# Kernel optimization log

Measured on AMD Instinct MI355X. Metric: run time of the kernel, lower is better.

The kernel has to match this reference:

```python
import jax, jax.numpy as jnp
import numpy as np

N_HEAD = 16
NEG_INF = -1e9  # matches the original's -1000000000.0 mask fill


def setup_inputs() -> dict:
    key = jax.random.key(0)
    k1, k2, k3 = jax.random.split(key, 3)
    n_embd = 1024
    b, t = 2, 2048
    x = jax.random.normal(k1, (b, t, n_embd), dtype=jnp.float32)
    w_attn = jax.random.normal(k2, (n_embd, 3 * n_embd), dtype=jnp.float32) * 0.02
    b_attn = jnp.zeros((3 * n_embd,), dtype=jnp.float32)
    w_proj = jax.random.normal(k3, (n_embd, n_embd), dtype=jnp.float32) * 0.02
    b_proj = jnp.zeros((n_embd,), dtype=jnp.float32)
    return {"x": x, "w_attn": w_attn, "b_attn": b_attn, "w_proj": w_proj, "b_proj": b_proj}


def reference(x, w_attn, b_attn, w_proj, b_proj):
    b, t, c = x.shape
    hd = c // N_HEAD
    scale = 1.0 / np.sqrt(hd)
    qkv = x @ w_attn + b_attn                        # [b, t, 3c]
    q, k, v = jnp.split(qkv, 3, axis=-1)
    # split heads -> [b, nh, t, hd]
    def heads(z):
        return z.reshape(b, t, N_HEAD, hd).transpose(0, 2, 1, 3)
    q, k, v = heads(q), heads(k), heads(v)
    att = jnp.einsum('bhqd,bhkd->bhqk', q, k) * scale  # [b, nh, t, t]
    mask = jnp.tril(jnp.ones((t, t), dtype=bool))
    att = jnp.where(mask[None, None], att, jnp.float32(NEG_INF))
    att = jax.nn.softmax(att, axis=-1)
    y = jnp.einsum('bhqk,bhkd->bhqd', att, v)          # [b, nh, t, hd]
    y = y.transpose(0, 2, 1, 3).reshape(b, t, c)
    return y @ w_proj + b_proj
```

## Files before the change

### kernel.cpp

```cpp
#include <hip/hip_runtime.h>
#include <hip/hip_bf16.h>
#include <math.h>

typedef __attribute__((ext_vector_type(8))) short short8;
typedef __attribute__((ext_vector_type(4))) float f32x4;
typedef unsigned short u16;

static __device__ __forceinline__ u16 f2bf(float f) {
  union { float f; unsigned u; } v; v.f = f;
  unsigned r = v.u + 0x7fffu + ((v.u >> 16) & 1u);
  return (u16)(r >> 16);
}

static __device__ __forceinline__ float bf2f(u16 h) {
  union { unsigned u; float f; } v; v.u = ((unsigned)h) << 16;
  return v.f;
}

static __device__ __forceinline__ void gload_lds16(const void* g, void* l) {
  __builtin_amdgcn_global_load_lds(
      (const __attribute__((address_space(1))) void*)g,
      (__attribute__((address_space(3))) void*)l, 16, 0, 0);
}

__global__ __launch_bounds__(256) void cvt_bf16(const float* __restrict__ in,
                                                u16* __restrict__ out, int n) {
  int i = (blockIdx.x * 256 + threadIdx.x) * 8;
  if (i >= n) return;
  float4 a = *(const float4*)(in + i);
  float4 b = *(const float4*)(in + i + 4);
  uint4 pk;
  pk.x = f2bf(a.x) | ((unsigned)f2bf(a.y) << 16);
  pk.y = f2bf(a.z) | ((unsigned)f2bf(a.w) << 16);
  pk.z = f2bf(b.x) | ((unsigned)f2bf(b.y) << 16);
  pk.w = f2bf(b.z) | ((unsigned)f2bf(b.w) << 16);
  *(uint4*)(out + i) = pk;
}

template<int KD, int ND>
__global__ __launch_bounds__(256) void transpose_bf16(const float* __restrict__ W,
                                                      u16* __restrict__ WT) {
  __shared__ float tile[64][65];
  const int c0 = blockIdx.x * 64;
  const int k0 = blockIdx.y * 64;
  const int t = threadIdx.x;
  const int lr = t >> 2;
  const int lc = (t & 3) * 16;
  const float* src = W + (size_t)(k0 + lr) * ND + c0 + lc;
#pragma unroll
  for (int i = 0; i < 16; i += 4) {
    float4 v = *(const float4*)(src + i);
    tile[lr][lc + i] = v.x; tile[lr][lc + i + 1] = v.y;
    tile[lr][lc + i + 2] = v.z; tile[lr][lc + i + 3] = v.w;
  }
  __syncthreads();
  unsigned pk[8];
#pragma unroll
  for (int j = 0; j < 8; ++j) {
    u16 lo = f2bf(tile[lc + 2 * j][lr]);
    u16 hi = f2bf(tile[lc + 2 * j + 1][lr]);
    pk[j] = lo | ((unsigned)hi << 16);
  }
  u16* dst = WT + (size_t)(c0 + lr) * KD + k0 + lc;
  *(uint4*)(dst) = make_uint4(pk[0], pk[1], pk[2], pk[3]);
  *(uint4*)(dst + 8) = make_uint4(pk[4], pk[5], pk[6], pk[7]);
}

template<int NSIZE, int MODE>
__global__ __launch_bounds__(256) void gemm_bt(const u16* __restrict__ A,
                                               const u16* __restrict__ Bt,
                                               const float* __restrict__ bias,
                                               u16* __restrict__ qb,
                                               u16* __restrict__ kb,
                                               u16* __restrict__ vb,
                                               float* __restrict__ outp) {
  constexpr int K = 1024;
  __shared__ u16 As[128 * 64];
  __shared__ u16 Bs[128 * 64];
  const int tid = threadIdx.x;
  const int lane = tid & 63;
  const int wid = tid >> 6;
  const int l15 = lane & 15;
  const int g4 = lane >> 4;
  const int wm = (wid >> 1) * 64;
  const int wn = (wid & 1) * 64;
  const int row0 = blockIdx.x * 128;
  const int col0 = blockIdx.y * 128;

  f32x4 acc[4][4] = {};

  const int srow = tid >> 3;
  const int sblk = (tid & 7) ^ (srow & 7);
  const u16* ga = A + (size_t)(row0 + srow) * K + sblk * 8;
  const u16* gb = Bt + (size_t)(col0 + srow) * K + sblk * 8;
  u16* la = As + tid * 8;
  u16* lb = Bs + tid * 8;

  for (int kt = 0; kt < K / 64; ++kt) {
#pragma unroll
    for (int i = 0; i < 4; ++i) {
      gload_lds16(ga + (size_t)i * 32 * K + kt * 64, la + i * 2048);
      gload_lds16(gb + (size_t)i * 32 * K + kt * 64, lb + i * 2048);
    }
    __syncthreads();
#pragma unroll
    for (int ks = 0; ks < 2; ++ks) {
      short8 af[4], bf[4];
      const int B = ks * 64 + g4 * 16;
      const int sw = (l15 & 7) << 4;
#pragma unroll
      for (int mt = 0; mt < 4; ++mt)
        af[mt] = *(const short8*)((const char*)As + (wm + mt * 16 + l15) * 128 + (B ^ sw));
#pragma unroll
      for (int nt = 0; nt < 4; ++nt)
        bf[nt] = *(const short8*)((const char*)Bs + (wn + nt * 16 + l15) * 128 + (B ^ sw));
#pragma unroll
      for (int mt = 0; mt < 4; ++mt)
#pragma unroll
        for (int nt = 0; nt < 4; ++nt)
          acc[mt][nt] = __builtin_amdgcn_mfma_f32_16x16x32_bf16(af[mt], bf[nt], acc[mt][nt], 0, 0, 0);
    }
    __syncthreads();
  }

#pragma unroll
  for (int nt = 0; nt < 4; ++nt) {
    const int col = col0 + wn + nt * 16 + l15;
    const float bv = bias[col];
    if (MODE == 0) {
      const int part = col >> 10;
      const int h = (col >> 6) & 15;
      const int d = col & 63;
      u16* dp = part == 0 ? qb : kb;
#pragma unroll
      for (int mt = 0; mt < 4; ++mt) {
        if (part == 2) {
          const int t0 = row0 + wm + mt * 16 + g4 * 4;
          const int bidx = t0 >> 11;
          const int tt = t0 & 2047;
          const unsigned lo = f2bf(acc[mt][nt][0] + bv) | ((unsigned)f2bf(acc[mt][nt][1] + bv) << 16);
          const unsigned hi = f2bf(acc[mt][nt][2] + bv) | ((unsigned)f2bf(acc[mt][nt][3] + bv) << 16);
          *(uint2*)&vb[((size_t)((bidx << 4) + h) * 64 + d) * 2048 + tt] = make_uint2(lo, hi);
        } else {
#pragma unroll
          for (int r = 0; r < 4; ++r) {
            const int row = row0 + wm + mt * 16 + g4 * 4 + r;
            const int bidx = row >> 11;
            const int tt = row & 2047;
            dp[((size_t)((bidx << 4) + h) * 2048 + tt) * 64 + d] = f2bf(acc[mt][nt][r] + bv);
          }
        }
      }
    } else {
#pragma unroll
      for (int mt = 0; mt < 4; ++mt) {
#pragma unroll
        for (int r = 0; r < 4; ++r) {
          const int row = row0 + wm + mt * 16 + g4 * 4 + r;
          outp[(size_t)row * NSIZE + col] = acc[mt][nt][r] + bv;
        }
      }
    }
  }
}

__global__ __launch_bounds__(256, 3) void attn_fwd(const u16* __restrict__ Qb,
                                                   const u16* __restrict__ Kb,
                                                   const u16* __restrict__ Vtb,
                                                   u16* __restrict__ Yb,
                                                   char* __restrict__ pb) {
  __shared__ u16 Ks[2][64 * 64];
  __shared__ u16 Vs[2][64 * 64];
  __shared__ u16 Ps[4][2048];
  const int bh = blockIdx.x;
  const int y = blockIdx.y;
  int j, c0t, c1t, chunk, split;
  if (y < 8)       { j = 8 + y;  c0t = 0;  c1t = 15;        chunk = 0; split = 1; }
  else if (y < 16) { j = 15 - y; c0t = 0;  c1t = 2 * j + 1; chunk = 0; split = 0; }
  else             { j = y - 8;  c0t = 16; c1t = 2 * j + 1; chunk = 1; split = 1; }
  const int q0 = j * 128;
  const int tid = threadIdx.x;
  const int lane = tid & 63;
  const int wid = tid >> 6;
  const int l15 = lane & 15;
  const int g4 = lane >> 4;
  const size_t bhq = (size_t)bh * 2048 * 64;
  const u16* Kbase = Kb + bhq;
  const u16* Vbase = Vtb + bhq;
  const float C2 = 0.18033688011112042f;
  u16* Pw = &Ps[wid][0];
  const int wrow0 = q0 + wid * 32;

  short8 ones;
#pragma unroll
  for (int i = 0; i < 8; ++i) ones[i] = (short)0x3F80;

  short8 qf[2][2];
#pragma unroll
  for (int g = 0; g < 2; ++g) {
    const u16* qp = Qb + bhq + (size_t)(wrow0 + g * 16 + l15) * 64 + g4 * 8;
    qf[g][0] = *(const short8*)(qp);
    qf[g][1] = *(const short8*)(qp + 32);
  }
  f32x4 accy[2][4] = {};
  float m_q[2] = {-1e30f, -1e30f};
  float m_r[2][4] = {{-1e30f, -1e30f, -1e30f, -1e30f}, {-1e30f, -1e30f, -1e30f, -1e30f}};
  float l_r[2][4] = {};

  int cur = 0;
#pragma unroll
  for (int cc = 0; cc < 2; ++cc) {
    const int c = tid + cc * 256;
    const int srow = c >> 3;
    const int sblk = (c & 7) ^ (srow & 7);
    gload_lds16(Kbase + (size_t)(c0t * 64 + srow) * 64 + sblk * 8, Ks[0] + c * 8);
    gload_lds16(Vbase + (size_t)srow * 2048 + c0t * 64 + sblk * 8, Vs[0] + c * 8);
  }

  for (int kv = c0t; kv <= c1t; ++kv) {
    const int kv0 = kv * 64;
    if (kv < c1t) {
      const int nx0 = kv0 + 64;
#pragma unroll
      for (int cc = 0; cc < 2; ++cc) {
        const int c = tid + cc * 256;
        const int srow = c >> 3;
        const int sblk = (c & 7) ^ (srow & 7);
        gload_lds16(Kbase + (size_t)(nx0 + srow) * 64 + sblk * 8, Ks[cur ^ 1] + c * 8);
        gload_lds16(Vbase + (size_t)srow * 2048 + nx0 + sblk * 8, Vs[cur ^ 1] + c * 8);
      }
      asm volatile("s_waitcnt vmcnt(4)" ::: "memory");
    } else {
      asm volatile("s_waitcnt vmcnt(0)" ::: "memory");
    }
    __builtin_amdgcn_s_barrier();
    asm volatile("" ::: "memory");

    if (kv0 <= wrow0 + 31) {
      const u16* Kt = Ks[cur];
      const u16* Vt = Vs[cur];

      f32x4 s[2][4];
#pragma unroll
      for (int nt = 0; nt < 4; ++nt) {
        const int R = nt * 16 + l15;
        const int sw = (R & 7) << 4;
        short8 kf0 = *(const short8*)((const char*)Kt + R * 128 + ((g4 * 16) ^ sw));
        short8 kf1 = *(const short8*)((const char*)Kt + R * 128 + ((64 + g4 * 16) ^ sw));
        f32x4 z0 = __builtin_amdgcn_mfma_f32_16x16x32_bf16(kf0, qf[0][0], f32x4{}, 0, 0, 0);
        s[0][nt] = __builtin_amdgcn_mfma_f32_16x16x32_bf16(kf1, qf[0][1], z0, 0, 0, 0);
        f32x4 z1 = __builtin_amdgcn_mfma_f32_16x16x32_bf16(kf0, qf[1][0], f32x4{}, 0, 0, 0);
        s[1][nt] = __builtin_amdgcn_mfma_f32_16x16x32_bf16(kf1, qf[1][1], z1, 0, 0, 0);
      }

#pragma unroll
      for (int g = 0; g < 2; ++g) {
        const int grow0 = wrow0 + g * 16;
        if (kv0 + 63 > grow0) {
          const int qg = grow0 + l15;
#pragma unroll
          for (int nt = 0; nt < 4; ++nt) {
            const int kbase = kv0 + nt * 16 + g4 * 4;
#pragma unroll
            for (int r = 0; r < 4; ++r)
              if (kbase + r > qg) s[g][nt][r] = -1e30f;
          }
        }
        float mx = fmaxf(fmaxf(fmaxf(s[g][0][0], s[g][0][1]), fmaxf(s[g][0][2], s[g][0][3])),
                         fmaxf(fmaxf(s[g][1][0], s[g][1][1]), fmaxf(s[g][1][2], s[g][1][3])));
        mx = fmaxf(mx, fmaxf(fmaxf(fmaxf(s[g][2][0], s[g][2][1]), fmaxf(s[g][2][2], s[g][2][3])),
                             fmaxf(fmaxf(s[g][3][0], s[g][3][1]), fmaxf(s[g][3][2], s[g][3][3]))));
        mx = fmaxf(mx, __shfl_xor(mx, 16));
        mx = fmaxf(mx, __shfl_xor(mx, 32));
        if (!__all(mx <= m_q[g] + 44.0f)) {
          m_q[g] = fmaxf(m_q[g], mx);
#pragma unroll
          for (int rr = 0; rr < 4; ++rr) {
            const float mn = __shfl(m_q[g], g4 * 4 + rr);
            const float al = __builtin_amdgcn_exp2f((m_r[g][rr] - mn) * C2);
            m_r[g][rr] = mn;
            l_r[g][rr] *= al;
#pragma unroll
            for (int nt = 0; nt < 4; ++nt) accy[g][nt][rr] *= al;
          }
        }
        const float m2 = m_q[g] * C2;
#pragma unroll
        for (int nt = 0; nt < 4; ++nt)
#pragma unroll
          for (int r = 0; r < 4; ++r)
            s[g][nt][r] = __builtin_amdgcn_exp2f(fmaf(s[g][nt][r], C2, -m2));

#pragma unroll
        for (int nt = 0; nt < 4; ++nt) {
          const unsigned lo = f2bf(s[g][nt][0]) | ((unsigned)f2bf(s[g][nt][1]) << 16);
          const unsigned hi = f2bf(s[g][nt][2]) | ((unsigned)f2bf(s[g][nt][3]) << 16);
          const int rowL = g * 16 + l15;
          const int colB = nt * 32 + g4 * 8;
          *(uint2*)((char*)Pw + rowL * 128 + (colB ^ ((rowL & 7) << 4))) = make_uint2(lo, hi);
        }
      }

      short8 pf[2][2];
#pragma unroll
      for (int g = 0; g < 2; ++g) {
        const int rowL = g * 16 + l15;
        const int sw = (rowL & 7) << 4;
        pf[g][0] = *(const short8*)((const char*)Pw + rowL * 128 + ((g4 * 16) ^ sw));
        pf[g][1] = *(const short8*)((const char*)Pw + rowL * 128 + ((64 + g4 * 16) ^ sw));
      }
#pragma unroll
      for (int g = 0; g < 2; ++g) {
        f32x4 ps = __builtin_amdgcn_mfma_f32_16x16x32_bf16(pf[g][0], ones, f32x4{}, 0, 0, 0);
        ps = __builtin_amdgcn_mfma_f32_16x16x32_bf16(pf[g][1], ones, ps, 0, 0, 0);
#pragma unroll
        for (int rr = 0; rr < 4; ++rr) l_r[g][rr] += ps[rr];
      }
#pragma unroll
      for (int nt = 0; nt < 4; ++nt) {
        const int R = nt * 16 + l15;
        const int sw = (R & 7) << 4;
        short8 vf0 = *(const short8*)((const char*)Vt + R * 128 + ((g4 * 16) ^ sw));
        short8 vf1 = *(const short8*)((const char*)Vt + R * 128 + ((64 + g4 * 16) ^ sw));
#pragma unroll
        for (int g = 0; g < 2; ++g) {
          accy[g][nt] = __builtin_amdgcn_mfma_f32_16x16x32_bf16(pf[g][0], vf0, accy[g][nt], 0, 0, 0);
          accy[g][nt] = __builtin_amdgcn_mfma_f32_16x16x32_bf16(pf[g][1], vf1, accy[g][nt], 0, 0, 0);
        }
      }
    }

    asm volatile("" ::: "memory");
    __builtin_amdgcn_s_barrier();
    cur ^= 1;
  }

  if (!split) {
#pragma unroll
    for (int g = 0; g < 2; ++g)
#pragma unroll
      for (int r = 0; r < 4; ++r) {
        const int row = wrow0 + g * 16 + g4 * 4 + r;
        const float inv = 1.0f / l_r[g][r];
        const size_t base = ((size_t)(bh >> 4) * 2048 + row) * 1024 + (bh & 15) * 64;
#pragma unroll
        for (int nt = 0; nt < 4; ++nt)
          Yb[base + nt * 16 + l15] = f2bf(accy[g][nt][r] * inv);
      }
  } else {
    char* slot = pb + ((size_t)(bh * 8 + (j - 8)) * 2 + chunk) * 17408;
    u16* O = (u16*)slot;
    float* mf = (float*)(slot + 16384);
    float* lf = (float*)(slot + 16896);
#pragma unroll
    for (int g = 0; g < 2; ++g)
#pragma unroll
      for (int r = 0; r < 4; ++r) {
        const int row = wid * 32 + g * 16 + g4 * 4 + r;
        const float inv = 1.0f / l_r[g][r];
#pragma unroll
        for (int nt = 0; nt < 4; ++nt)
          O[row * 64 + nt * 16 + l15] = f2bf(accy[g][nt][r] * inv);
        if (l15 == 0) { mf[row] = m_r[g][r]; lf[row] = l_r[g][r]; }
      }
  }
}

__global__ __launch_bounds__(256) void attn_combine(const char* __restrict__ pb,
                                                    u16* __restrict__ Yb) {
  const int x = blockIdx.x;
  const int bh = blockIdx.y;
  const int j = 8 + (x >> 1);
  const int half = x & 1;
  const int T = 2 * j + half;
  const char* s0 = pb + ((size_t)(bh * 8 + (j - 8)) * 2) * 17408;
  const char* s1 = s0 + 17408;
  const int tid = threadIdx.x;
  const int r64 = tid >> 2;
  const int rowl = half * 64 + r64;
  const int dc = (tid & 3) * 16;
  const float C2 = 0.18033688011112042f;
  const float m0 = ((const float*)(s0 + 16384))[rowl];
  const float m1 = ((const float*)(s1 + 16384))[rowl];
  const float l0 = ((const float*)(s0 + 16896))[rowl];
  const float l1 = ((const float*)(s1 + 16896))[rowl];
  const float m = fmaxf(m0, m1);
  const float w0 = __builtin_amdgcn_exp2f((m0 - m) * C2) * l0;
  const float w1 = __builtin_amdgcn_exp2f((m1 - m) * C2) * l1;
  const float inv = 1.0f / (w0 + w1);
  const float a0 = w0 * inv, a1 = w1 * inv;
  const u16* O0 = (const u16*)s0 + rowl * 64 + dc;
  const u16* O1 = (const u16*)s1 + rowl * 64 + dc;
  const int qrow = T * 64 + r64;
  u16* yp = Yb + ((size_t)(bh >> 4) * 2048 + qrow) * 1024 + (bh & 15) * 64 + dc;
  union { uint4 v; u16 h[8]; } a[2], b[2], o[2];
  a[0].v = *(const uint4*)O0; a[1].v = *(const uint4*)(O0 + 8);
  b[0].v = *(const uint4*)O1; b[1].v = *(const uint4*)(O1 + 8);
#pragma unroll
  for (int jj = 0; jj < 2; ++jj)
#pragma unroll
    for (int i = 0; i < 8; ++i)
      o[jj].h[i] = f2bf(bf2f(a[jj].h[i]) * a0 + bf2f(b[jj].h[i]) * a1);
  *(uint4*)yp = o[0].v;
  *(uint4*)(yp + 8) = o[1].v;
}

extern "C" void kernel_launch(void* const* d_in, const int* in_sizes, int n_in,
                              void* d_out, int out_size, void* d_ws, size_t ws_size,
                              hipStream_t stream) {
  const float* x      = (const float*)d_in[0];
  const float* w_attn = (const float*)d_in[1];
  const float* b_attn = (const float*)d_in[2];
  const float* w_proj = (const float*)d_in[3];
  const float* b_proj = (const float*)d_in[4];
  float* out = (float*)d_out;
  char* ws = (char*)d_ws;

  u16* xb  = (u16*)(ws + (size_t)0);
  u16* wTa = (u16*)(ws + ((size_t)8  << 20));
  u16* wTp = (u16*)(ws + ((size_t)14 << 20));
  u16* qb  = (u16*)(ws + ((size_t)16 << 20));
  u16* kb  = (u16*)(ws + ((size_t)24 << 20));
  u16* vb  = (u16*)(ws + ((size_t)32 << 20));
  u16* yb  = (u16*)(ws + ((size_t)40 << 20));
  char* pb = ws;

  cvt_bf16<<<2048, 256, 0, stream>>>(x, xb, 2 * 2048 * 1024);
  transpose_bf16<1024, 3072><<<dim3(48, 16), 256, 0, stream>>>(w_attn, wTa);
  transpose_bf16<1024, 1024><<<dim3(16, 16), 256, 0, stream>>>(w_proj, wTp);
  gemm_bt<3072, 0><<<dim3(32, 24), 256, 0, stream>>>(xb, wTa, b_attn, qb, kb, vb, nullptr);
  attn_fwd<<<dim3(32, 24), 256, 0, stream>>>(qb, kb, vb, yb, pb);
  attn_combine<<<dim3(16, 32), 256, 0, stream>>>(pb, yb);
  gemm_bt<1024, 1><<<dim3(32, 8), 256, 0, stream>>>(yb, wTp, b_proj, nullptr, nullptr, nullptr, out);
}
```

Measured before the change: 125.2 us.

## Double-buffer LDS tiles in GEMM to overlap global loads with MFMA

```diff
diff --git a/kernel.cpp b/kernel.cpp
--- a/kernel.cpp
+++ b/kernel.cpp
@@ -75,8 +75,8 @@
                                                u16* __restrict__ vb,
                                                float* __restrict__ outp) {
   constexpr int K = 1024;
-  __shared__ u16 As[128 * 64];
-  __shared__ u16 Bs[128 * 64];
+  __shared__ u16 As[2][128 * 64];
+  __shared__ u16 Bs[2][128 * 64];
   const int tid = threadIdx.x;
   const int lane = tid & 63;
   const int wid = tid >> 6;
@@ -93,16 +93,30 @@
   const int sblk = (tid & 7) ^ (srow & 7);
   const u16* ga = A + (size_t)(row0 + srow) * K + sblk * 8;
   const u16* gb = Bt + (size_t)(col0 + srow) * K + sblk * 8;
-  u16* la = As + tid * 8;
-  u16* lb = Bs + tid * 8;
-
+
+#pragma unroll
+  for (int i = 0; i < 4; ++i) {
+    gload_lds16(ga + (size_t)i * 32 * K, As[0] + tid * 8 + i * 2048);
+    gload_lds16(gb + (size_t)i * 32 * K, Bs[0] + tid * 8 + i * 2048);
+  }
+
+  int cur = 0;
   for (int kt = 0; kt < K / 64; ++kt) {
-#pragma unroll
-    for (int i = 0; i < 4; ++i) {
-      gload_lds16(ga + (size_t)i * 32 * K + kt * 64, la + i * 2048);
-      gload_lds16(gb + (size_t)i * 32 * K + kt * 64, lb + i * 2048);
+    if (kt + 1 < K / 64) {
+#pragma unroll
+      for (int i = 0; i < 4; ++i) {
+        gload_lds16(ga + (size_t)i * 32 * K + (kt + 1) * 64, As[cur ^ 1] + tid * 8 + i * 2048);
+        gload_lds16(gb + (size_t)i * 32 * K + (kt + 1) * 64, Bs[cur ^ 1] + tid * 8 + i * 2048);
+      }
+      asm volatile("s_waitcnt vmcnt(8)" ::: "memory");
+    } else {
+      asm volatile("s_waitcnt vmcnt(0)" ::: "memory");
     }
-    __syncthreads();
+    __builtin_amdgcn_s_barrier();
+    asm volatile("" ::: "memory");
+
+    const u16* Ac = As[cur];
+    const u16* Bc = Bs[cur];
 #pragma unroll
     for (int ks = 0; ks < 2; ++ks) {
       short8 af[4], bf[4];
@@ -110,17 +124,20 @@
       const int sw = (l15 & 7) << 4;
 #pragma unroll
       for (int mt = 0; mt < 4; ++mt)
-        af[mt] = *(const short8*)((const char*)As + (wm + mt * 16 + l15) * 128 + (B ^ sw));
+        af[mt] = *(const short8*)((const char*)Ac + (wm + mt * 16 + l15) * 128 + (B ^ sw));
 #pragma unroll
       for (int nt = 0; nt < 4; ++nt)
-        bf[nt] = *(const short8*)((const char*)Bs + (wn + nt * 16 + l15) * 128 + (B ^ sw));
+        bf[nt] = *(const short8*)((const char*)Bc + (wn + nt * 16 + l15) * 128 + (B ^ sw));
 #pragma unroll
       for (int mt = 0; mt < 4; ++mt)
 #pragma unroll
         for (int nt = 0; nt < 4; ++nt)
           acc[mt][nt] = __builtin_amdgcn_mfma_f32_16x16x32_bf16(af[mt], bf[nt], acc[mt][nt], 0, 0, 0);
     }
-    __syncthreads();
+
+    asm volatile("" ::: "memory");
+    __builtin_amdgcn_s_barrier();
+    cur ^= 1;
   }
 
 #pragma unroll
```

Result: no change. 123.0 us (-1.7%).
